# Kernel tuning notes

Hardware: AMD Instinct MI355X
Metric: run time of the kernel (lower is better)

The kernel has to match this reference:

```python
import jax, jax.numpy as jnp
import numpy as np

V, B, NT, EN, EMB, ODIM = 5000, 512, 50, 200, 200, 40
PERP = 30.0
BETA_TEMP = 0.2
SINKHORN_ALPHA = 20.0
WEIGHT_ECR = 250.0
ECR_ITERS = 100
SNE_ITERS = 20
EPS_DIV = 1e-16


def _pairwise_sq(x, y):
    # ||x_i||^2 + ||y_j||^2 - 2 x_i . y_j  (matches module's pairwise_euclidean_distance)
    return (jnp.sum(x * x, axis=1)[:, None] + jnp.sum(y * y, axis=1)[None, :]
            - 2.0 * (x @ y.T))


def _bn_train(x, g, b):
    # BatchNorm1d, training mode: batch statistics, biased variance
    m = x.mean(axis=0)
    v = x.var(axis=0)
    return (x - m) / jnp.sqrt(v + 1e-5) * g + b


def _snekhorn_reduce(X, proj):
    # SNEkhorn-style symmetric entropic affinity on rows of X (log-domain
    # symmetric Sinkhorn with uniform marginals), followed by a linear readout
    # to ODIM dims. X: (n, d) -> (n, ODIM).
    C = _pairwise_sq(X, X)                       # (n, n)
    n = X.shape[0]
    eps = jnp.mean(C) / jnp.log(PERP) + 1e-6     # bandwidth tied to perplexity
    log_a = -jnp.log(float(n))                   # uniform target marginal

    @jax.checkpoint
    def step(f, _):
        lse = jax.nn.logsumexp((f[None, :] - C) / eps, axis=1)
        f = 0.5 * (f + eps * (log_a - lse))      # symmetric Sinkhorn update
        return f, None

    f, _ = jax.lax.scan(step, jnp.zeros(n, C.dtype), None, length=SNE_ITERS)
    P = jnp.exp((f[:, None] + f[None, :] - C) / eps)  # (n, n) affinity
    return P @ proj                                   # (n, ODIM)


def _ecr_loss(cost):
    # ECR: entropic OT between topic and word embeddings (fixed-iteration Sinkhorn)
    Km = jnp.exp(-cost * SINKHORN_ALPHA)          # (NT, V)
    a = jnp.full((NT, 1), 1.0 / NT, cost.dtype)
    bm = jnp.full((V, 1), 1.0 / V, cost.dtype)

    def step(u, _):
        v = bm / (Km.T @ u + EPS_DIV)
        u = a / (Km @ v + EPS_DIV)
        return u, None

    u, _ = jax.lax.scan(step, jnp.full((NT, 1), 1.0 / NT, cost.dtype), None,
                        length=ECR_ITERS)
    v = bm / (Km.T @ u + EPS_DIV)
    transp = u * (Km * v.T)
    return WEIGHT_ECR * jnp.sum(transp * cost)


def setup_inputs() -> dict:
    key = jax.random.key(0)
    ks = jax.random.split(key, 12)

    def nrm(k, shape, s=0.02):
        return jax.random.normal(k, shape, jnp.float32) * s

    word_emb = jax.random.normal(ks[0], (V, EMB), jnp.float32)
    word_emb = word_emb / jnp.linalg.norm(word_emb, axis=1, keepdims=True)
    topic_emb = jax.random.normal(ks[1], (NT, EMB), jnp.float32) * 0.1
    topic_emb = topic_emb / jnp.linalg.norm(topic_emb, axis=1, keepdims=True)

    return dict(
        bow=jax.random.uniform(ks[2], (B, V), jnp.float32),
        eps_noise=jax.random.normal(ks[3], (ODIM, NT), jnp.float32),
        W1=nrm(ks[4], (EN, V)), b1=jnp.zeros(EN, jnp.float32),
        W2=nrm(ks[5], (EN, EN)), b2=jnp.zeros(EN, jnp.float32),
        Wmu=nrm(ks[6], (NT, EN)), bmu=jnp.zeros(NT, jnp.float32),
        Wlv=nrm(ks[7], (NT, EN)), blv=jnp.zeros(NT, jnp.float32),
        g_mu=jnp.ones(NT, jnp.float32), be_mu=jnp.zeros(NT, jnp.float32),
        g_lv=jnp.ones(NT, jnp.float32), be_lv=jnp.zeros(NT, jnp.float32),
        g_dec=jnp.ones(V, jnp.float32), be_dec=jnp.zeros(V, jnp.float32),
        word_emb=word_emb, topic_emb=topic_emb,
        proj_V=nrm(ks[8], (V, ODIM), 1.0),
        proj_K=nrm(ks[9], (NT, ODIM), 1.0),
    )


def reference(bow, eps_noise, W1, b1, W2, b2, Wmu, bmu, Wlv, blv,
              g_mu, be_mu, g_lv, be_lv, g_dec, be_dec,
              word_emb, topic_emb, proj_V, proj_K):
    # bow_reduced = SNEkhorn(bow.T).T : (ODIM, V)
    bow_reduced = _snekhorn_reduce(bow.T, proj_V).T

    # encoder1: Linear -> softplus -> Linear -> softplus
    e1 = jax.nn.softplus(bow_reduced @ W1.T + b1)
    e1 = jax.nn.softplus(e1 @ W2.T + b2)
    mu = _bn_train(e1 @ Wmu.T + bmu, g_mu, be_mu)        # (ODIM, NT)
    logvar = _bn_train(e1 @ Wlv.T + blv, g_lv, be_lv)

    z = mu + eps_noise * jnp.exp(0.5 * logvar)           # reparameterize (training)
    theta = jax.nn.softmax(z, axis=1)                    # (ODIM, NT)
    theta_reduced = _snekhorn_reduce(theta.T, proj_K).T  # (ODIM, NT)

    # KL vs logistic-normal prior; with a = ones: mu2 = 0, var2 = 1 - 1/NT
    var2 = 1.0 - 1.0 / NT
    var = jnp.exp(logvar)
    kld = 0.5 * ((var / var2 + mu * mu / var2 + jnp.log(var2) - logvar).sum(axis=1) - NT)
    loss_KL = kld.mean()

    # beta + decode (cost computed once; torch code computes it twice identically)
    cost = _pairwise_sq(topic_emb, word_emb)             # (NT, V)
    beta = jax.nn.softmax(-cost / BETA_TEMP, axis=0)
    recon = jax.nn.softmax(_bn_train(theta_reduced @ beta, g_dec, be_dec), axis=-1)
    recon_loss = -(bow_reduced * jnp.log(recon)).sum(axis=1).mean()

    loss_TM = recon_loss + loss_KL
    loss_ECR = _ecr_loss(cost)
    loss = loss_TM + loss_ECR
    return loss, loss_TM, loss_ECR, theta_reduced
```

## Files before the change

### kernel.cpp

```cpp
#include <hip/hip_runtime.h>
#include <hip/hip_bf16.h>
#include <hip/hip_fp16.h>

#define VV 5000
#define NTOP 50
#define ENH 200
#define NEMB 200
#define OD 40
#define MP 5120
#define KNS 5008

typedef __attribute__((ext_vector_type(8))) short short8;
typedef __attribute__((ext_vector_type(4))) float f32x4;

constexpr size_t OFF_R      = 0;
constexpr size_t OFF_S      = 20224;
constexpr size_t OFF_SCAL   = 22528;
constexpr size_t OFF_PHIA   = 22784;
constexpr size_t OFF_PHIB   = 43008;
constexpr size_t OFF_ROWS   = 63232;
constexpr size_t OFF_PARTS  = 63744;
constexpr size_t OFF_FLAGS  = 71936;
constexpr size_t OFF_MUPRE  = 72960;
constexpr size_t OFF_LVPRE  = 81152;
constexpr size_t OFF_E1T    = 89344;
constexpr size_t OFF_E2T    = 121600;
constexpr size_t OFF_THRED  = 153856;
constexpr size_t OFF_BOWRED = 162048;
constexpr size_t ZERO_BYTES = 962304;
constexpr size_t OFF_PVT    = 962304;
constexpr size_t OFF_XB     = 1453824;
constexpr size_t OFF_CE     = 6696704;
constexpr size_t OFF_COST   = 56696832;
constexpr size_t OFF_KM     = 57697024;
constexpr size_t OFF_BETA   = 58697216;
constexpr size_t OFF_RN     = 59697408;

__global__ __launch_bounds__(256) void k1_stats(const float* __restrict__ bow,
    __hip_bfloat16* __restrict__ Xb, float* __restrict__ r, float* __restrict__ s){
  __shared__ float lds[64][129];
  const int t = threadIdx.x;
  const int i0 = blockIdx.x * 128, d0 = blockIdx.y * 64;
  #pragma unroll
  for (int m = 0; m < 32; ++m){
    int idx = m*256 + t;
    int di = idx >> 7;
    int ii = idx & 127;
    int gi = i0 + ii;
    lds[di][ii] = (gi < VV) ? bow[(size_t)(d0+di)*VV + gi] : 0.f;
  }
  __syncthreads();
  if (t < 128 && (i0 + t) < VV){
    float acc = 0.f;
    for (int di = 0; di < 64; ++di){ float v = lds[di][t]; acc += v*v; }
    atomicAdd(&r[i0+t], acc);
  }
  if (t < 64){
    float acc = 0.f;
    for (int ii = 0; ii < 128; ++ii) acc += lds[t][ii];
    atomicAdd(&s[d0+t], acc);
  }
  __syncthreads();
  #pragma unroll
  for (int m = 0; m < 32; ++m){
    int idx = m*256 + t;
    int ii = idx >> 6;
    int dd = idx & 63;
    Xb[(size_t)(i0+ii)*512 + d0 + dd] = __float2bfloat16(lds[dd][ii]);
  }
}

__global__ __launch_bounds__(256) void k2_eps(const float* __restrict__ r,
    const float* __restrict__ s, float* __restrict__ scal){
  const int t = threadIdx.x;
  float a = 0.f, b = 0.f;
  for (int i = t; i < VV; i += 256) a += r[i];
  for (int d = t; d < 512; d += 256){ float v = s[d]; b += v*v; }
  #pragma unroll
  for (int off = 32; off; off >>= 1){
    a += __shfl_down(a, off, 64);
    b += __shfl_down(b, off, 64);
  }
  __shared__ float ra[4], rb[4];
  int lane = t & 63, w = t >> 6;
  if (lane == 0){ ra[w] = a; rb[w] = b; }
  __syncthreads();
  if (t == 0){
    float sa = ra[0]+ra[1]+ra[2]+ra[3];
    float sb = rb[0]+rb[1]+rb[2]+rb[3];
    float meanC = 2.f*sa/(float)VV - 2.f*sb/((float)VV*(float)VV);
    float eps = meanC / logf(30.f) + 1e-6f;
    scal[0] = eps;
    scal[1] = 1.f/eps;
  }
}

__device__ __forceinline__ void ecr_block(int b, int it_base, int n_iters, bool do_final,
    const __half* __restrict__ Kn, const float* __restrict__ cost,
    float* __restrict__ acc, int* __restrict__ cnt, float* __restrict__ scal,
    char* smem){
  __half* KmL = (__half*)smem;
  float* varr = (float*)(smem + 32208);
  float* us   = (float*)(smem + 33488);
  float* p5   = (float*)(smem + 33696);
  float* redr = (float*)(smem + 34736);
  const int t = threadIdx.x;
  const int base = (b < 8) ? b*313 : 2504 + (b-8)*312;
  const int sz   = (b < 8) ? 313 : 312;
  for (int c = t; c < 322; c += 256){
    if (c < sz){
      #pragma unroll
      for (int q = 0; q < NTOP; ++q)
        KmL[q*322 + c] = Kn[(size_t)q*KNS + base + c];
    } else {
      #pragma unroll
      for (int q = 0; q < NTOP; ++q) KmL[q*322 + c] = __float2half(0.f);
    }
  }
  if (t < 52){
    float u0 = 0.f;
    if (t < NTOP){
      if (it_base == 0) u0 = 1.f/(float)NTOP;
      else {
        float sm = __hip_atomic_load(&acc[((it_base-1)%3)*64 + t],
                                     __ATOMIC_RELAXED, __HIP_MEMORY_SCOPE_AGENT);
        u0 = (1.f/(float)NTOP)/(sm + 1e-16f);
      }
    }
    us[t] = u0;
  }
  for (int c = sz + t; c < 320; c += 256) varr[c] = 0.f;
  __syncthreads();
  const bool act = (2*t < sz);
  for (int k = 0; k < n_iters; ++k){
    const int g = it_base + k;
    if (act){
      float w0 = 0.f, w1 = 0.f, w2 = 0.f, w3 = 0.f;
      #pragma unroll
      for (int q = 0; q < NTOP; q += 2){
        float u0 = us[q], u1 = us[q+1];
        float2 f0 = __half22float2(*(const __half2*)(KmL + q*322 + 2*t));
        float2 f1 = __half22float2(*(const __half2*)(KmL + (q+1)*322 + 2*t));
        w0 += f0.x*u0; w1 += f0.y*u0;
        w2 += f1.x*u1; w3 += f1.y*u1;
      }
      float2 vv;
      vv.x = (1.f/(float)VV)/((w0+w2) + 1e-16f);
      vv.y = (2*t+1 < sz) ? (1.f/(float)VV)/((w1+w3) + 1e-16f) : 0.f;
      *(float2*)(varr + 2*t) = vv;
    }
    __syncthreads();
    if (t < 250){
      const int qq = t % NTOP, stripe = t / NTOP;
      const __half* kp = KmL + qq*322 + stripe*64;
      const float* vp = varr + stripe*64;
      float s0 = 0.f, s1 = 0.f, s2 = 0.f, s3 = 0.f;
      #pragma unroll
      for (int n = 0; n < 64; n += 4){
        float2 fa = __half22float2(*(const __half2*)(kp + n));
        float2 fb = __half22float2(*(const __half2*)(kp + n + 2));
        float4 v4 = *(const float4*)(vp + n);
        s0 += fa.x*v4.x; s1 += fa.y*v4.y; s2 += fb.x*v4.z; s3 += fb.y*v4.w;
      }
      p5[stripe*52 + qq] = (s0+s1)+(s2+s3);
    }
    __syncthreads();
    if (t < NTOP){
      float sm = p5[t] + p5[52+t] + p5[104+t] + p5[156+t] + p5[208+t];
      __hip_atomic_fetch_add(&acc[(g%3)*64 + t], sm,
                             __ATOMIC_RELAXED, __HIP_MEMORY_SCOPE_AGENT);
    }
    __asm__ volatile("s_waitcnt vmcnt(0)" ::: "memory");
    if (t == 0){
      __hip_atomic_fetch_add(cnt, 1, __ATOMIC_RELEASE, __HIP_MEMORY_SCOPE_AGENT);
      const int tgt = 16*(g+1);
      while (__hip_atomic_load(cnt, __ATOMIC_ACQUIRE, __HIP_MEMORY_SCOPE_AGENT) < tgt)
        __builtin_amdgcn_s_sleep(1);
    }
    if (t < NTOP){
      float sm = __hip_atomic_load(&acc[(g%3)*64 + t],
                                   __ATOMIC_RELAXED, __HIP_MEMORY_SCOPE_AGENT);
      us[t] = (1.f/(float)NTOP)/(sm + 1e-16f);
    }
    if (t < 64)
      __hip_atomic_store(&acc[((g+2)%3)*64 + t], 0.f,
                         __ATOMIC_RELAXED, __HIP_MEMORY_SCOPE_AGENT);
    __syncthreads();
  }
  if (!do_final) return;
  float lsum = 0.f;
  if (act){
    float w0 = 0.f, w1 = 0.f, w2 = 0.f, w3 = 0.f;
    #pragma unroll
    for (int q = 0; q < NTOP; q += 2){
      float u0 = us[q], u1 = us[q+1];
      float2 f0 = __half22float2(*(const __half2*)(KmL + q*322 + 2*t));
      float2 f1 = __half22float2(*(const __half2*)(KmL + (q+1)*322 + 2*t));
      w0 += f0.x*u0; w1 += f0.y*u0;
      w2 += f1.x*u1; w3 += f1.y*u1;
    }
    float v0 = (1.f/(float)VV)/((w0+w2) + 1e-16f);
    const bool ok1 = (2*t+1 < sz);
    float v1 = ok1 ? (1.f/(float)VV)/((w1+w3) + 1e-16f) : 0.f;
    float accv = 0.f;
    #pragma unroll
    for (int q = 0; q < NTOP; ++q){
      float2 f = __half22float2(*(const __half2*)(KmL + q*322 + 2*t));
      float uq = us[q];
      float c0 = cost[(size_t)q*VV + base + 2*t];
      accv += uq*f.x*v0*c0;
      if (ok1){
        float c1 = cost[(size_t)q*VV + base + 2*t + 1];
        accv += uq*f.y*v1*c1;
      }
    }
    lsum = accv;
  }
  #pragma unroll
  for (int off = 32; off; off >>= 1) lsum += __shfl_down(lsum, off, 64);
  if ((t & 63) == 0) redr[t >> 6] = lsum;
  __syncthreads();
  if (t == 0) atomicAdd(&scal[3], redr[0]+redr[1]+redr[2]+redr[3]);
}

__global__ __launch_bounds__(256) void k3_gemm_ecr(const __hip_bfloat16* __restrict__ Xb,
    const float* __restrict__ r, float* __restrict__ scal, __half* __restrict__ Ce,
    const __half* __restrict__ Kn, const float* __restrict__ cost,
    float* __restrict__ accg, int* __restrict__ cnt){
  __shared__ __align__(16) char smem[36864];
  if (blockIdx.x < 16){
    ecr_block(blockIdx.x, 0, 12, false, Kn, cost, accg, cnt, scal, smem);
    return;
  }
  __hip_bfloat16* As = (__hip_bfloat16*)smem;
  __hip_bfloat16* Bs = (__hip_bfloat16*)(smem + 128*72*2);
  const int b2 = blockIdx.x - 16;
  const int t = threadIdx.x;
  const int i0 = (b2 % 40) * 128, j0 = (b2 / 40) * 128;
  const int lane = t & 63, w = t >> 6;
  const int wr = w >> 1, wc = w & 1;
  const int m16 = lane & 15, q4 = lane >> 4;
  f32x4 acc[4][4];
  #pragma unroll
  for (int a = 0; a < 4; ++a)
    #pragma unroll
    for (int b = 0; b < 4; ++b) acc[a][b] = (f32x4){0.f,0.f,0.f,0.f};
  const int srow = t >> 3, sseg = t & 7;
  for (int kc = 0; kc < 512; kc += 64){
    __syncthreads();
    #pragma unroll
    for (int m = 0; m < 4; ++m){
      int row = m*32 + srow;
      uint4 va = *(const uint4*)(Xb + (size_t)(i0+row)*512 + kc + sseg*8);
      *(uint4*)(As + row*72 + sseg*8) = va;
      uint4 vb = *(const uint4*)(Xb + (size_t)(j0+row)*512 + kc + sseg*8);
      *(uint4*)(Bs + row*72 + sseg*8) = vb;
    }
    __syncthreads();
    #pragma unroll
    for (int ks = 0; ks < 64; ks += 32){
      short8 af[4], bf[4];
      #pragma unroll
      for (int f = 0; f < 4; ++f){
        af[f] = *(const short8*)(As + (wr*64 + f*16 + m16)*72 + ks + q4*8);
        bf[f] = *(const short8*)(Bs + (wc*64 + f*16 + m16)*72 + ks + q4*8);
      }
      #pragma unroll
      for (int fr = 0; fr < 4; ++fr)
        #pragma unroll
        for (int fc = 0; fc < 4; ++fc)
          acc[fr][fc] = __builtin_amdgcn_mfma_f32_16x16x32_bf16(af[fr], bf[fc], acc[fr][fc], 0, 0, 0);
    }
  }
  const float inv_eps = scal[1];
  #pragma unroll
  for (int fr = 0; fr < 4; ++fr){
    int rbase = i0 + wr*64 + fr*16 + q4*4;
    #pragma unroll
    for (int fc = 0; fc < 4; ++fc){
      int col = j0 + wc*64 + fc*16 + m16;
      if (col < VV){
        float rc = r[col];
        #pragma unroll
        for (int q = 0; q < 4; ++q){
          int row = rbase + q;
          if (row < VV){
            float val = (r[row] + rc - 2.f*acc[fr][fc][q]) * inv_eps;
            Ce[(size_t)row*VV + col] = __float2half(val);
          }
        }
      }
    }
  }
}

__global__ __launch_bounds__(256) void k4_sweep_ecr(const __half* __restrict__ Ce,
    const float* __restrict__ phi_in, float* __restrict__ phi_out,
    const __half* __restrict__ Kn, const float* __restrict__ cost,
    float* __restrict__ accg, int* __restrict__ cnt, float* __restrict__ scal,
    int it_base, int n_ecr){
  __shared__ __align__(16) char smem[34752];
  const int t = threadIdx.x;
  if (blockIdx.x < 16){
    ecr_block(blockIdx.x, it_base, n_ecr, it_base + n_ecr == 100,
              Kn, cost, accg, cnt, scal, smem);
    return;
  }
  const int i0 = (blockIdx.x - 16) * 4;
  float acc[4] = {0.f, 0.f, 0.f, 0.f};
  const uint4* ce0 = (const uint4*)(Ce + (size_t)i0*VV);
  for (int u = t; u < 625; u += 256){
    float4 p0 = *(const float4*)(phi_in + u*8);
    float4 p1 = *(const float4*)(phi_in + u*8 + 4);
    #pragma unroll
    for (int rr = 0; rr < 4; ++rr){
      uint4 v = ce0[(size_t)rr*625 + u];
      const __half2* hp = (const __half2*)&v;
      float2 c0 = __half22float2(hp[0]);
      float2 c1 = __half22float2(hp[1]);
      float2 c2 = __half22float2(hp[2]);
      float2 c3 = __half22float2(hp[3]);
      acc[rr] += __expf(p0.x - c0.x) + __expf(p0.y - c0.y)
               + __expf(p0.z - c1.x) + __expf(p0.w - c1.y)
               + __expf(p1.x - c2.x) + __expf(p1.y - c2.y)
               + __expf(p1.z - c3.x) + __expf(p1.w - c3.y);
    }
  }
  #pragma unroll
  for (int rr = 0; rr < 4; ++rr)
    #pragma unroll
    for (int off = 32; off; off >>= 1)
      acc[rr] += __shfl_down(acc[rr], off, 64);
  float* red = (float*)smem;
  int lane = t & 63, w = t >> 6;
  if (lane == 0){
    #pragma unroll
    for (int rr = 0; rr < 4; ++rr) red[w*4 + rr] = acc[rr];
  }
  __syncthreads();
  if (t < 4){
    float ssum = red[t] + red[4+t] + red[8+t] + red[12+t];
    const float loga = -8.517193191416238f;
    phi_out[i0 + t] = 0.5f*(phi_in[i0 + t] + loga - __logf(ssum));
  }
}

__global__ __launch_bounds__(256) void k5p_pvt(const float* __restrict__ projV,
    __hip_bfloat16* __restrict__ pvt){
  int idx = blockIdx.x*256 + threadIdx.x;
  if (idx >= 48*MP) return;
  int n = idx / MP, j = idx - n*MP;
  float v = (n < OD && j < VV) ? projV[(size_t)j*OD + n] : 0.f;
  pvt[idx] = __float2bfloat16(v);
}

__global__ __launch_bounds__(256) void k5_bowred(const __half* __restrict__ Ce,
    const float* __restrict__ phi, const __hip_bfloat16* __restrict__ pvt,
    float* __restrict__ brpA, float* __restrict__ brpB){
  __shared__ __align__(16) char smem[25600];
  __hip_bfloat16* As = (__hip_bfloat16*)smem;
  __hip_bfloat16* Bs = (__hip_bfloat16*)(smem + 18432);
  const int t = threadIdx.x;
  const int i0 = blockIdx.x * 128;
  const int k0 = blockIdx.y * 640;
  const int lane = t & 63, w = t >> 6;
  const int m16 = lane & 15, q4 = lane >> 4;
  f32x4 acc[2][3];
  #pragma unroll
  for (int a = 0; a < 2; ++a)
    #pragma unroll
    for (int b = 0; b < 3; ++b) acc[a][b] = (f32x4){0.f,0.f,0.f,0.f};
  for (int kc = k0; kc < k0 + 640; kc += 64){
    __syncthreads();
    #pragma unroll
    for (int m = 0; m < 4; ++m){
      int g = m*256 + t;
      int row = g >> 3, cg = g & 7;
      int gi = i0 + row, j2 = kc + cg*8;
      union { __hip_bfloat16 h[8]; short8 v; } u;
      if (gi < VV && j2 < VV){
        uint4 vce = *(const uint4*)(Ce + (size_t)gi*VV + j2);
        const __half2* hp = (const __half2*)&vce;
        float pb = phi[gi];
        float4 pj0 = *(const float4*)(phi + j2);
        float4 pj1 = *(const float4*)(phi + j2 + 4);
        float pj[8] = {pj0.x,pj0.y,pj0.z,pj0.w,pj1.x,pj1.y,pj1.z,pj1.w};
        #pragma unroll
        for (int e = 0; e < 4; ++e){
          float2 ce = __half22float2(hp[e]);
          u.h[2*e]   = __float2bfloat16(__expf(pb + pj[2*e]   - ce.x));
          u.h[2*e+1] = __float2bfloat16(__expf(pb + pj[2*e+1] - ce.y));
        }
      } else {
        #pragma unroll
        for (int e = 0; e < 8; ++e) u.h[e] = __float2bfloat16(0.f);
      }
      *(short8*)(As + row*72 + cg*8) = u.v;
    }
    #pragma unroll
    for (int m = 0; m < 12; ++m){
      int idx = m*256 + t;
      int row = idx >> 6, c = idx & 63;
      Bs[row*72 + c] = pvt[(size_t)row*MP + kc + c];
    }
    __syncthreads();
    #pragma unroll
    for (int ks = 0; ks < 64; ks += 32){
      short8 af[2], bf[3];
      #pragma unroll
      for (int f = 0; f < 2; ++f)
        af[f] = *(const short8*)(As + (w*32 + f*16 + m16)*72 + ks + q4*8);
      #pragma unroll
      for (int f = 0; f < 3; ++f)
        bf[f] = *(const short8*)(Bs + (f*16 + m16)*72 + ks + q4*8);
      #pragma unroll
      for (int fr = 0; fr < 2; ++fr)
        #pragma unroll
        for (int fc = 0; fc < 3; ++fc)
          acc[fr][fc] = __builtin_amdgcn_mfma_f32_16x16x32_bf16(af[fr], bf[fc], acc[fr][fc], 0, 0, 0);
    }
  }
  __syncthreads();
  float* LF = (float*)smem;
  #pragma unroll
  for (int fr = 0; fr < 2; ++fr){
    int lr = w*32 + fr*16 + q4*4;
    #pragma unroll
    for (int fc = 0; fc < 3; ++fc){
      int col = fc*16 + m16;
      #pragma unroll
      for (int q = 0; q < 4; ++q)
        LF[col*133 + lr + q] = acc[fr][fc][q];
    }
  }
  __syncthreads();
  float* brp = (blockIdx.y < 6) ? brpA + (size_t)blockIdx.y*200000
                                : brpB + (size_t)(blockIdx.y - 6)*200000;
  for (int o = t; o < OD*128; o += 256){
    int col = o >> 7, row = o & 127;
    int gr = i0 + row;
    if (gr < VV) brp[(size_t)col*VV + gr] = LF[col*133 + row];
  }
}

__global__ __launch_bounds__(256) void k5r_red(const float* __restrict__ brpA,
    const float* __restrict__ brpB, float* __restrict__ br){
  int idx = blockIdx.x*256 + threadIdx.x;
  if (idx >= 50000) return;
  const float4* a = (const float4*)brpA;
  const float4* b = (const float4*)brpB;
  float4 s = a[idx];
  #pragma unroll
  for (int sl = 1; sl < 6; ++sl){
    float4 v = a[(size_t)sl*50000 + idx];
    s.x += v.x; s.y += v.y; s.z += v.z; s.w += v.w;
  }
  #pragma unroll
  for (int sl = 0; sl < 2; ++sl){
    float4 v = b[(size_t)sl*50000 + idx];
    s.x += v.x; s.y += v.y; s.z += v.z; s.w += v.w;
  }
  ((float4*)br)[idx] = s;
}

__global__ __launch_bounds__(256) void k6_e1(const float* __restrict__ br,
    const float* __restrict__ W1, float* __restrict__ e1pre){
  const int t = threadIdx.x;
  const int lane = t & 63, w = t >> 6;
  const int k = blockIdx.x*4 + w;
  const int f0 = blockIdx.y * 125;
  float acc[OD];
  #pragma unroll
  for (int i = 0; i < OD; ++i) acc[i] = 0.f;
  const float4* w4p = (const float4*)(W1 + (size_t)k*VV);
  for (int f4 = f0 + lane; f4 < f0 + 125; f4 += 64){
    float4 wv = w4p[f4];
    #pragma unroll
    for (int i = 0; i < OD; ++i){
      float4 bv = ((const float4*)(br + (size_t)i*VV))[f4];
      acc[i] += bv.x*wv.x + bv.y*wv.y + bv.z*wv.z + bv.w*wv.w;
    }
  }
  #pragma unroll
  for (int i = 0; i < OD; ++i)
    #pragma unroll
    for (int off = 32; off; off >>= 1)
      acc[i] += __shfl_down(acc[i], off, 64);
  __shared__ float red[4][OD];
  if (lane == 0){
    #pragma unroll
    for (int i = 0; i < OD; ++i) red[w][i] = acc[i];
  }
  __syncthreads();
  if (t < 160){
    int ww = t / OD, i = t - ww*OD;
    int kk = blockIdx.x*4 + ww;
    atomicAdd(&e1pre[kk*OD + i], red[ww][i]);
  }
}

__global__ __launch_bounds__(256) void k6b_sp(const float* __restrict__ b1,
    float* __restrict__ e1t){
  int idx = blockIdx.x*256 + threadIdx.x;
  if (idx >= ENH*OD) return;
  int kk = idx / OD;
  float x = e1t[idx] + b1[kk];
  e1t[idx] = (x > 20.f) ? x : log1pf(__expf(x));
}

__global__ __launch_bounds__(256) void k7_e2(const float* __restrict__ e1t,
    const float* __restrict__ W2, const float* __restrict__ b2, float* __restrict__ e2t){
  const int t = threadIdx.x;
  const int lane = t & 63, w = t >> 6;
  const int k = blockIdx.x*4 + w;
  float acc[OD];
  #pragma unroll
  for (int i = 0; i < OD; ++i) acc[i] = 0.f;
  for (int j = lane; j < ENH; j += 64){
    float wv = W2[(size_t)k*ENH + j];
    #pragma unroll
    for (int i = 0; i < OD; ++i) acc[i] += e1t[j*OD + i] * wv;
  }
  #pragma unroll
  for (int i = 0; i < OD; ++i)
    #pragma unroll
    for (int off = 32; off; off >>= 1)
      acc[i] += __shfl_down(acc[i], off, 64);
  __shared__ float red[4][OD];
  if (lane == 0){
    #pragma unroll
    for (int i = 0; i < OD; ++i) red[w][i] = acc[i];
  }
  __syncthreads();
  if (t < 160){
    int ww = t / OD, i = t - ww*OD;
    int kk = blockIdx.x*4 + ww;
    float x = red[ww][i] + b2[kk];
    float sp = (x > 20.f) ? x : log1pf(__expf(x));
    e2t[kk*OD + i] = sp;
  }
}

__global__ __launch_bounds__(256) void k8a_mulv(const float* __restrict__ e2t,
    const float* __restrict__ Wmu, const float* __restrict__ bmu,
    const float* __restrict__ Wlv, const float* __restrict__ blv,
    float* __restrict__ mupre, float* __restrict__ lvpre){
  int id = blockIdx.x*256 + threadIdx.x;
  if (id >= NTOP*OD) return;
  int t50 = id / OD, i = id - t50*OD;
  float am = 0.f, al = 0.f;
  for (int kk = 0; kk < ENH; ++kk){
    float e = e2t[kk*OD + i];
    am += e * Wmu[t50*ENH + kk];
    al += e * Wlv[t50*ENH + kk];
  }
  mupre[t50*OD + i] = am + bmu[t50];
  lvpre[t50*OD + i] = al + blv[t50];
}

__global__ __launch_bounds__(256) void k8b_theta(const float* __restrict__ mupre,
    const float* __restrict__ lvpre,
    const float* __restrict__ g_mu, const float* __restrict__ be_mu,
    const float* __restrict__ g_lv, const float* __restrict__ be_lv,
    const float* __restrict__ eps_noise, const float* __restrict__ projK,
    float* __restrict__ thred, float* __restrict__ d_out3, float* __restrict__ scal){
  __shared__ float mu[NTOP][OD];
  __shared__ float lv[NTOP][OD];
  __shared__ float th[OD][NTOP];
  __shared__ float C2[NTOP][NTOP];
  __shared__ float P2[NTOP][NTOP];
  __shared__ float f2[NTOP], nf[NTOP];
  __shared__ float sred[4];
  __shared__ float eps2s[2];
  const int t = threadIdx.x;
  if (t < NTOP){
    float m = 0.f;
    for (int i = 0; i < OD; ++i) m += mupre[t*OD + i];
    m *= (1.f/OD);
    float v = 0.f;
    for (int i = 0; i < OD; ++i){ float d = mupre[t*OD+i] - m; v += d*d; }
    v *= (1.f/OD);
    float sc = g_mu[t] * rsqrtf(v + 1e-5f);
    float sh = be_mu[t];
    for (int i = 0; i < OD; ++i) mu[t][i] = (mupre[t*OD+i] - m)*sc + sh;
    m = 0.f;
    for (int i = 0; i < OD; ++i) m += lvpre[t*OD + i];
    m *= (1.f/OD);
    v = 0.f;
    for (int i = 0; i < OD; ++i){ float d = lvpre[t*OD+i] - m; v += d*d; }
    v *= (1.f/OD);
    sc = g_lv[t] * rsqrtf(v + 1e-5f);
    sh = be_lv[t];
    for (int i = 0; i < OD; ++i) lv[t][i] = (lvpre[t*OD+i] - m)*sc + sh;
  }
  __syncthreads();
  {
    float kl = 0.f;
    if (t < OD){
      const float var2 = 1.f - 1.f/(float)NTOP;
      const float lv2 = logf(var2);
      float ssum = 0.f;
      for (int q = 0; q < NTOP; ++q){
        float l = lv[q][t];
        float m = mu[q][t];
        ssum += (__expf(l) + m*m)/var2 + lv2 - l;
      }
      kl = 0.5f*(ssum - (float)NTOP);
    }
    #pragma unroll
    for (int off = 32; off; off >>= 1) kl += __shfl_down(kl, off, 64);
    if ((t & 63) == 0) sred[t >> 6] = kl;
    __syncthreads();
    if (t == 0) scal[2] = (sred[0]+sred[1]+sred[2]+sred[3]) * (1.f/OD);
    __syncthreads();
  }
  if (t < OD){
    float z[NTOP];
    float mx = -1e30f;
    for (int q = 0; q < NTOP; ++q){
      float val = mu[q][t] + eps_noise[t*NTOP + q]*__expf(0.5f*lv[q][t]);
      z[q] = val;
      mx = fmaxf(mx, val);
    }
    float ssum = 0.f;
    for (int q = 0; q < NTOP; ++q){ float e = __expf(z[q]-mx); z[q] = e; ssum += e; }
    float inv = 1.f/ssum;
    for (int q = 0; q < NTOP; ++q) th[t][q] = z[q]*inv;
  }
  __syncthreads();
  {
    float csum = 0.f;
    for (int pr = t; pr < NTOP*NTOP; pr += 256){
      int a = pr / NTOP, b = pr - (pr/NTOP)*NTOP;
      float ss = 0.f;
      for (int i = 0; i < OD; ++i){ float d = th[i][a] - th[i][b]; ss += d*d; }
      C2[a][b] = ss;
      csum += ss;
    }
    #pragma unroll
    for (int off = 32; off; off >>= 1) csum += __shfl_down(csum, off, 64);
    if ((t & 63) == 0) sred[t >> 6] = csum;
    __syncthreads();
    if (t == 0){
      float meanC = (sred[0]+sred[1]+sred[2]+sred[3]) / ((float)NTOP*NTOP);
      float e2 = meanC / logf(30.f) + 1e-6f;
      eps2s[0] = e2; eps2s[1] = 1.f/e2;
    }
  }
  if (t < NTOP) f2[t] = 0.f;
  __syncthreads();
  const float loga2 = -logf((float)NTOP);
  for (int it = 0; it < 20; ++it){
    if (t < NTOP){
      float ie = eps2s[1];
      float ssum = 0.f;
      for (int sI = 0; sI < NTOP; ++sI)
        ssum += __expf((f2[sI] - C2[t][sI]) * ie);
      float lse = __logf(ssum);
      nf[t] = 0.5f*(f2[t] + eps2s[0]*(loga2 - lse));
    }
    __syncthreads();
    if (t < NTOP) f2[t] = nf[t];
    __syncthreads();
  }
  for (int pr = t; pr < NTOP*NTOP; pr += 256){
    int a = pr / NTOP, b = pr - (pr/NTOP)*NTOP;
    P2[a][b] = __expf((f2[a] + f2[b] - C2[a][b]) * eps2s[1]);
  }
  __syncthreads();
  for (int o = t; o < NTOP*OD; o += 256){
    int t50 = o / OD, kk = o - (o/OD)*OD;
    float ssum = 0.f;
    for (int sI = 0; sI < NTOP; ++sI)
      ssum += P2[t50][sI] * projK[sI*OD + kk];
    thred[kk*NTOP + t50] = ssum;
    d_out3[kk*NTOP + t50] = ssum;
  }
}

__global__ __launch_bounds__(256) void k10_cost(const float* __restrict__ temb,
    const float* __restrict__ wemb, float* __restrict__ cost, __half* __restrict__ Kn,
    float* __restrict__ beta){
  __shared__ float Tt[100][52];
  __shared__ float wed[100][68];
  __shared__ float sc[52][64];
  __shared__ float tn[52];
  __shared__ float wn[64];
  const int t = threadIdx.x;
  const int j0 = blockIdx.x * 64;
  const int tg = t >> 4, jg = t & 15;
  float am[4][4];
  #pragma unroll
  for (int a = 0; a < 4; ++a)
    #pragma unroll
    for (int b = 0; b < 4; ++b) am[a][b] = 0.f;
  float tnp = 0.f, wnp = 0.f;
  for (int c = 0; c < 2; ++c){
    __syncthreads();
    const int dbase = c*100;
    for (int idx = t; idx < NTOP*100; idx += 256){
      int t50 = idx / 100, d = idx - t50*100;
      Tt[d][t50] = temb[t50*NEMB + dbase + d];
    }
    for (int idx = t; idx < 64*100; idx += 256){
      int j = idx / 100, d = idx - j*100;
      int gj = j0 + j;
      wed[d][j] = (gj < VV) ? wemb[(size_t)gj*NEMB + dbase + d] : 0.f;
    }
    __syncthreads();
    if (t < NTOP){
      float a = 0.f;
      for (int d = 0; d < 100; ++d){ float v = Tt[d][t]; a += v*v; }
      tnp += a;
    }
    if (t >= 64 && t < 128){
      int j = t - 64;
      float a = 0.f;
      for (int d = 0; d < 100; ++d){ float v = wed[d][j]; a += v*v; }
      wnp += a;
    }
    if (t < 208){
      for (int d = 0; d < 100; ++d){
        const float4 tv = *(const float4*)(&Tt[d][tg*4]);
        const float4 wv = *(const float4*)(&wed[d][jg*4]);
        am[0][0] += tv.x*wv.x; am[0][1] += tv.x*wv.y; am[0][2] += tv.x*wv.z; am[0][3] += tv.x*wv.w;
        am[1][0] += tv.y*wv.x; am[1][1] += tv.y*wv.y; am[1][2] += tv.y*wv.z; am[1][3] += tv.y*wv.w;
        am[2][0] += tv.z*wv.x; am[2][1] += tv.z*wv.y; am[2][2] += tv.z*wv.z; am[2][3] += tv.z*wv.w;
        am[3][0] += tv.w*wv.x; am[3][1] += tv.w*wv.y; am[3][2] += tv.w*wv.z; am[3][3] += tv.w*wv.w;
      }
    }
  }
  if (t < NTOP) tn[t] = tnp;
  if (t >= 64 && t < 128) wn[t-64] = wnp;
  __syncthreads();
  if (t < 208){
    #pragma unroll
    for (int a = 0; a < 4; ++a){
      int t50 = tg*4 + a;
      if (t50 < NTOP){
        float tv = tn[t50];
        float cc[4];
        #pragma unroll
        for (int b = 0; b < 4; ++b) cc[b] = tv + wn[jg*4+b] - 2.f*am[a][b];
        int gj = j0 + jg*4;
        if (gj + 3 < VV)
          *(float4*)(cost + (size_t)t50*VV + gj) = make_float4(cc[0],cc[1],cc[2],cc[3]);
        #pragma unroll
        for (int b = 0; b < 4; ++b) sc[t50][jg*4+b] = -5.f*cc[b];
      }
    }
  }
  __syncthreads();
  if (t < 64){
    int gj = j0 + t;
    if (gj < VV){
      float mx = -1e30f;
      for (int q = 0; q < NTOP; ++q) mx = fmaxf(mx, sc[q][t]);
      float ssum = 0.f;
      for (int q = 0; q < NTOP; ++q){ float e = __expf(sc[q][t]-mx); sc[q][t] = e; ssum += e; }
      float inv = 1.f/ssum;
      for (int q = 0; q < NTOP; ++q){
        float e = sc[q][t];
        float e2 = e*e;
        Kn[(size_t)q*KNS + gj] = __float2half(e2*e2);
        beta[(size_t)q*VV + gj] = e*inv;
      }
    }
  }
}

__global__ __launch_bounds__(256) void k12_reconA(const float* __restrict__ thred,
    const float* __restrict__ beta, const float* __restrict__ g_dec,
    const float* __restrict__ be_dec, float* __restrict__ Rn){
  __shared__ float trs[OD][NTOP];
  const int t = threadIdx.x;
  for (int o = t; o < OD*NTOP; o += 256) trs[o/NTOP][o - (o/NTOP)*NTOP] = thred[o];
  __syncthreads();
  int j = blockIdx.x*256 + t;
  if (j >= VV) return;
  float a[OD];
  #pragma unroll
  for (int i = 0; i < OD; ++i) a[i] = 0.f;
  for (int q = 0; q < NTOP; ++q){
    float bv = beta[(size_t)q*VV + j];
    #pragma unroll
    for (int i = 0; i < OD; ++i) a[i] += trs[i][q]*bv;
  }
  float m = 0.f;
  #pragma unroll
  for (int i = 0; i < OD; ++i) m += a[i];
  m *= (1.f/OD);
  float v = 0.f;
  #pragma unroll
  for (int i = 0; i < OD; ++i){ float d = a[i]-m; v += d*d; }
  v *= (1.f/OD);
  float scale = g_dec[j]*rsqrtf(v + 1e-5f);
  float sh = be_dec[j];
  #pragma unroll
  for (int i = 0; i < OD; ++i) Rn[(size_t)i*VV + j] = (a[i]-m)*scale + sh;
}

__global__ __launch_bounds__(256) void k13_reconB(const float* __restrict__ Rn,
    const float* __restrict__ br, float* __restrict__ rows){
  const int i = blockIdx.x;
  const int t = threadIdx.x;
  float s1 = 0.f, s2 = 0.f, s3 = 0.f;
  for (int j = t; j < VV; j += 256){
    float rn = Rn[(size_t)i*VV + j];
    float bv = br[(size_t)i*VV + j];
    s1 += __expf(rn);
    s2 += bv*rn;
    s3 += bv;
  }
  #pragma unroll
  for (int off = 32; off; off >>= 1){
    s1 += __shfl_down(s1, off, 64);
    s2 += __shfl_down(s2, off, 64);
    s3 += __shfl_down(s3, off, 64);
  }
  __shared__ float red[3][4];
  int lane = t & 63, w = t >> 6;
  if (lane == 0){ red[0][w] = s1; red[1][w] = s2; red[2][w] = s3; }
  __syncthreads();
  if (t == 0){
    rows[i]      = red[0][0]+red[0][1]+red[0][2]+red[0][3];
    rows[40 + i] = red[1][0]+red[1][1]+red[1][2]+red[1][3];
    rows[80 + i] = red[2][0]+red[2][1]+red[2][2]+red[2][3];
  }
}

__global__ void k14_final(const float* __restrict__ rows, const float* __restrict__ scal,
    float* __restrict__ out){
  const int t = threadIdx.x;
  float v = 0.f;
  if (t < OD) v = rows[40 + t] - logf(rows[t]) * rows[80 + t];
  #pragma unroll
  for (int off = 32; off; off >>= 1) v += __shfl_down(v, off, 64);
  if (t == 0){
    float recon = -v * (1.f/OD);
    float tm = recon + scal[2];
    float ecr = 250.f * scal[3];
    out[0] = tm + ecr;
    out[1] = tm;
    out[2] = ecr;
  }
}

extern "C" void kernel_launch(void* const* d_in, const int* in_sizes, int n_in,
                              void* d_out, int out_size, void* d_ws, size_t ws_size,
                              hipStream_t stream){
  const float* bow   = (const float*)d_in[0];
  const float* epsn  = (const float*)d_in[1];
  const float* W1    = (const float*)d_in[2];
  const float* b1    = (const float*)d_in[3];
  const float* W2    = (const float*)d_in[4];
  const float* b2    = (const float*)d_in[5];
  const float* Wmu   = (const float*)d_in[6];
  const float* bmu   = (const float*)d_in[7];
  const float* Wlv   = (const float*)d_in[8];
  const float* blv   = (const float*)d_in[9];
  const float* g_mu  = (const float*)d_in[10];
  const float* be_mu = (const float*)d_in[11];
  const float* g_lv  = (const float*)d_in[12];
  const float* be_lv = (const float*)d_in[13];
  const float* g_dec = (const float*)d_in[14];
  const float* be_dec= (const float*)d_in[15];
  const float* wemb  = (const float*)d_in[16];
  const float* temb  = (const float*)d_in[17];
  const float* projV = (const float*)d_in[18];
  const float* projK = (const float*)d_in[19];
  char* ws = (char*)d_ws;
  float* r     = (float*)(ws + OFF_R);
  float* s     = (float*)(ws + OFF_S);
  float* scal  = (float*)(ws + OFF_SCAL);
  float* phiA  = (float*)(ws + OFF_PHIA);
  float* phiB  = (float*)(ws + OFF_PHIB);
  float* rows  = (float*)(ws + OFF_ROWS);
  float* accg  = (float*)(ws + OFF_PARTS);
  int*   cnt   = (int*)(ws + OFF_FLAGS);
  float* mupre = (float*)(ws + OFF_MUPRE);
  float* lvpre = (float*)(ws + OFF_LVPRE);
  float* e1t   = (float*)(ws + OFF_E1T);
  float* e2t   = (float*)(ws + OFF_E2T);
  float* thred = (float*)(ws + OFF_THRED);
  float* br    = (float*)(ws + OFF_BOWRED);
  __hip_bfloat16* pvt = (__hip_bfloat16*)(ws + OFF_PVT);
  __hip_bfloat16* Xb  = (__hip_bfloat16*)(ws + OFF_XB);
  __half* Ce   = (__half*)(ws + OFF_CE);
  float* cost  = (float*)(ws + OFF_COST);
  __half* Kn   = (__half*)(ws + OFF_KM);
  float* beta  = (float*)(ws + OFF_BETA);
  float* Rn    = (float*)(ws + OFF_RN);
  float* brpA  = (float*)(ws + OFF_XB);
  float* brpB  = (float*)(ws + OFF_COST);
  float* out   = (float*)d_out;

  hipMemsetAsync(d_ws, 0, ZERO_BYTES, stream);
  k10_cost<<<79, 256, 0, stream>>>(temb, wemb, cost, Kn, beta);
  k1_stats<<<dim3(40, 8), 256, 0, stream>>>(bow, Xb, r, s);
  k2_eps<<<1, 256, 0, stream>>>(r, s, scal);
  k3_gemm_ecr<<<1616, 256, 0, stream>>>(Xb, r, scal, Ce, Kn, cost, accg, cnt);
  {
    float* pin = phiA; float* pout = phiB;
    int itb = 12;
    for (int itr = 0; itr < 20; ++itr){
      int n = (itr < 12) ? 4 : 5;
      k4_sweep_ecr<<<1266, 256, 0, stream>>>(Ce, pin, pout, Kn, cost, accg, cnt,
                                             scal, itb, n);
      itb += n;
      float* tmp = pin; pin = pout; pout = tmp;
    }
  }
  k5p_pvt<<<960, 256, 0, stream>>>(projV, pvt);
  k5_bowred<<<dim3(40, 8), 256, 0, stream>>>(Ce, phiA, pvt, brpA, brpB);
  k5r_red<<<196, 256, 0, stream>>>(brpA, brpB, br);
  k6_e1<<<dim3(50, 10), 256, 0, stream>>>(br, W1, e1t);
  k6b_sp<<<32, 256, 0, stream>>>(b1, e1t);
  k7_e2<<<50, 256, 0, stream>>>(e1t, W2, b2, e2t);
  k8a_mulv<<<8, 256, 0, stream>>>(e2t, Wmu, bmu, Wlv, blv, mupre, lvpre);
  k8b_theta<<<1, 256, 0, stream>>>(mupre, lvpre, g_mu, be_mu, g_lv, be_lv,
                                   epsn, projK, thred, out + 3, scal);
  k12_reconA<<<20, 256, 0, stream>>>(thred, beta, g_dec, be_dec, Rn);
  k13_reconB<<<40, 256, 0, stream>>>(Rn, br, rows);
  k14_final<<<1, 64, 0, stream>>>(rows, scal, out);
}
```

Baseline: 845.8 us.

## Run ECR Sinkhorn in a single block with transposed Km, drop cross-block spin sync

Replaces the 16-block ECR Sinkhorn, which synchronised every iteration through global atomics and spin-waits, with a single block that streams a transposed (V x 52) half-precision Km and reduces through registers and LDS. The iterations are redistributed: 10 run in k1_stats, 20 in k3, and 3-4 in each sweep launch. The sweep kernel now handles 8 rows per block instead of 4, which halves its grid. The cost matrix is also stored transposed for the final loss term. The risk is that one block re-reading about 500KB from L2 per iteration could become the critical path inside each launch.

After: 1.777 ms. +110.1%, slower.

```diff
diff --git a/kernel.cpp b/kernel.cpp
--- a/kernel.cpp
+++ b/kernel.cpp
@@ -8,7 +8,6 @@
 #define NEMB 200
 #define OD 40
 #define MP 5120
-#define KNS 5008
 
 typedef __attribute__((ext_vector_type(8))) short short8;
 typedef __attribute__((ext_vector_type(4))) float f32x4;
@@ -19,8 +18,7 @@
 constexpr size_t OFF_PHIA   = 22784;
 constexpr size_t OFF_PHIB   = 43008;
 constexpr size_t OFF_ROWS   = 63232;
-constexpr size_t OFF_PARTS  = 63744;
-constexpr size_t OFF_FLAGS  = 71936;
+constexpr size_t OFF_UG     = 63744;
 constexpr size_t OFF_MUPRE  = 72960;
 constexpr size_t OFF_LVPRE  = 81152;
 constexpr size_t OFF_E1T    = 89344;
@@ -31,15 +29,93 @@
 constexpr size_t OFF_PVT    = 962304;
 constexpr size_t OFF_XB     = 1453824;
 constexpr size_t OFF_CE     = 6696704;
-constexpr size_t OFF_COST   = 56696832;
-constexpr size_t OFF_KM     = 57697024;
+constexpr size_t OFF_COSTT  = 56696832;
+constexpr size_t OFF_KNT    = 57736832;
 constexpr size_t OFF_BETA   = 58697216;
 constexpr size_t OFF_RN     = 59697408;
 
+__device__ __forceinline__ void ecr1(int it_base, int n_iters, bool do_final,
+    const __half* __restrict__ KnT, const float* __restrict__ costT,
+    float* __restrict__ ug, float* __restrict__ scal, char* smem){
+  float* us = (float*)smem;
+  float* pL = (float*)smem + 52;
+  const int t = threadIdx.x;
+  const int lane = t & 63, w = t >> 6;
+  if (t < 52) us[t] = (t < NTOP) ? ((it_base == 0) ? (1.f/(float)NTOP) : ug[t]) : 0.f;
+  __syncthreads();
+  for (int k = 0; k < n_iters; ++k){
+    float partial[52];
+    #pragma unroll
+    for (int q = 0; q < 52; ++q) partial[q] = 0.f;
+    for (int j = t; j < VV; j += 256){
+      const __half2* kp = (const __half2*)(KnT + (size_t)j*52);
+      float kf[52];
+      float w0 = 0.f;
+      #pragma unroll
+      for (int e = 0; e < 26; ++e){
+        float2 f = __half22float2(kp[e]);
+        kf[2*e] = f.x; kf[2*e+1] = f.y;
+        w0 += f.x*us[2*e] + f.y*us[2*e+1];
+      }
+      float vj = (1.f/(float)VV)/(w0 + 1e-16f);
+      #pragma unroll
+      for (int q = 0; q < 52; ++q) partial[q] += kf[q]*vj;
+    }
+    #pragma unroll
+    for (int q = 0; q < 52; ++q){
+      #pragma unroll
+      for (int off = 32; off; off >>= 1)
+        partial[q] += __shfl_down(partial[q], off, 64);
+    }
+    if (lane == 0){
+      #pragma unroll
+      for (int q = 0; q < 52; ++q) pL[w*52 + q] = partial[q];
+    }
+    __syncthreads();
+    if (t < NTOP){
+      float sm = pL[t] + pL[52+t] + pL[104+t] + pL[156+t];
+      us[t] = (1.f/(float)NTOP)/(sm + 1e-16f);
+    }
+    __syncthreads();
+  }
+  if (t < NTOP) ug[t] = us[t];
+  if (!do_final) return;
+  float lsum = 0.f;
+  for (int j = t; j < VV; j += 256){
+    const __half2* kp = (const __half2*)(KnT + (size_t)j*52);
+    float kf[52];
+    float w0 = 0.f;
+    #pragma unroll
+    for (int e = 0; e < 26; ++e){
+      float2 f = __half22float2(kp[e]);
+      kf[2*e] = f.x; kf[2*e+1] = f.y;
+      w0 += f.x*us[2*e] + f.y*us[2*e+1];
+    }
+    float vj = (1.f/(float)VV)/(w0 + 1e-16f);
+    const float* cp = costT + (size_t)j*52;
+    float a = 0.f;
+    #pragma unroll
+    for (int q = 0; q < NTOP; ++q)
+      a += us[q]*kf[q]*cp[q];
+    lsum += a*vj;
+  }
+  #pragma unroll
+  for (int off = 32; off; off >>= 1) lsum += __shfl_down(lsum, off, 64);
+  if (lane == 0) pL[w*52] = lsum;
+  __syncthreads();
+  if (t == 0) atomicAdd(&scal[3], pL[0] + pL[52] + pL[104] + pL[156]);
+}
+
 __global__ __launch_bounds__(256) void k1_stats(const float* __restrict__ bow,
-    __hip_bfloat16* __restrict__ Xb, float* __restrict__ r, float* __restrict__ s){
+    __hip_bfloat16* __restrict__ Xb, float* __restrict__ r, float* __restrict__ s,
+    const __half* __restrict__ KnT, const float* __restrict__ costT,
+    float* __restrict__ ug, float* __restrict__ scal){
   __shared__ float lds[64][129];
   const int t = threadIdx.x;
+  if (blockIdx.x == 40){
+    if (blockIdx.y == 0) ecr1(0, 10, false, KnT, costT, ug, scal, (char*)lds);
+    return;
+  }
   const int i0 = blockIdx.x * 128, d0 = blockIdx.y * 64;
   #pragma unroll
   for (int m = 0; m < 32; ++m){
@@ -95,146 +171,18 @@
   }
 }
 
-__device__ __forceinline__ void ecr_block(int b, int it_base, int n_iters, bool do_final,
-    const __half* __restrict__ Kn, const float* __restrict__ cost,
-    float* __restrict__ acc, int* __restrict__ cnt, float* __restrict__ scal,
-    char* smem){
-  __half* KmL = (__half*)smem;
-  float* varr = (float*)(smem + 32208);
-  float* us   = (float*)(smem + 33488);
-  float* p5   = (float*)(smem + 33696);
-  float* redr = (float*)(smem + 34736);
-  const int t = threadIdx.x;
-  const int base = (b < 8) ? b*313 : 2504 + (b-8)*312;
-  const int sz   = (b < 8) ? 313 : 312;
-  for (int c = t; c < 322; c += 256){
-    if (c < sz){
-      #pragma unroll
-      for (int q = 0; q < NTOP; ++q)
-        KmL[q*322 + c] = Kn[(size_t)q*KNS + base + c];
-    } else {
-      #pragma unroll
-      for (int q = 0; q < NTOP; ++q) KmL[q*322 + c] = __float2half(0.f);
-    }
-  }
-  if (t < 52){
-    float u0 = 0.f;
-    if (t < NTOP){
-      if (it_base == 0) u0 = 1.f/(float)NTOP;
-      else {
-        float sm = __hip_atomic_load(&acc[((it_base-1)%3)*64 + t],
-                                     __ATOMIC_RELAXED, __HIP_MEMORY_SCOPE_AGENT);
-        u0 = (1.f/(float)NTOP)/(sm + 1e-16f);
-      }
-    }
-    us[t] = u0;
-  }
-  for (int c = sz + t; c < 320; c += 256) varr[c] = 0.f;
-  __syncthreads();
-  const bool act = (2*t < sz);
-  for (int k = 0; k < n_iters; ++k){
-    const int g = it_base + k;
-    if (act){
-      float w0 = 0.f, w1 = 0.f, w2 = 0.f, w3 = 0.f;
-      #pragma unroll
-      for (int q = 0; q < NTOP; q += 2){
-        float u0 = us[q], u1 = us[q+1];
-        float2 f0 = __half22float2(*(const __half2*)(KmL + q*322 + 2*t));
-        float2 f1 = __half22float2(*(const __half2*)(KmL + (q+1)*322 + 2*t));
-        w0 += f0.x*u0; w1 += f0.y*u0;
-        w2 += f1.x*u1; w3 += f1.y*u1;
-      }
-      float2 vv;
-      vv.x = (1.f/(float)VV)/((w0+w2) + 1e-16f);
-      vv.y = (2*t+1 < sz) ? (1.f/(float)VV)/((w1+w3) + 1e-16f) : 0.f;
-      *(float2*)(varr + 2*t) = vv;
-    }
-    __syncthreads();
-    if (t < 250){
-      const int qq = t % NTOP, stripe = t / NTOP;
-      const __half* kp = KmL + qq*322 + stripe*64;
-      const float* vp = varr + stripe*64;
-      float s0 = 0.f, s1 = 0.f, s2 = 0.f, s3 = 0.f;
-      #pragma unroll
-      for (int n = 0; n < 64; n += 4){
-        float2 fa = __half22float2(*(const __half2*)(kp + n));
-        float2 fb = __half22float2(*(const __half2*)(kp + n + 2));
-        float4 v4 = *(const float4*)(vp + n);
-        s0 += fa.x*v4.x; s1 += fa.y*v4.y; s2 += fb.x*v4.z; s3 += fb.y*v4.w;
-      }
-      p5[stripe*52 + qq] = (s0+s1)+(s2+s3);
-    }
-    __syncthreads();
-    if (t < NTOP){
-      float sm = p5[t] + p5[52+t] + p5[104+t] + p5[156+t] + p5[208+t];
-      __hip_atomic_fetch_add(&acc[(g%3)*64 + t], sm,
-                             __ATOMIC_RELAXED, __HIP_MEMORY_SCOPE_AGENT);
-    }
-    __asm__ volatile("s_waitcnt vmcnt(0)" ::: "memory");
-    if (t == 0){
-      __hip_atomic_fetch_add(cnt, 1, __ATOMIC_RELEASE, __HIP_MEMORY_SCOPE_AGENT);
-      const int tgt = 16*(g+1);
-      while (__hip_atomic_load(cnt, __ATOMIC_ACQUIRE, __HIP_MEMORY_SCOPE_AGENT) < tgt)
-        __builtin_amdgcn_s_sleep(1);
-    }
-    if (t < NTOP){
-      float sm = __hip_atomic_load(&acc[(g%3)*64 + t],
-                                   __ATOMIC_RELAXED, __HIP_MEMORY_SCOPE_AGENT);
-      us[t] = (1.f/(float)NTOP)/(sm + 1e-16f);
-    }
-    if (t < 64)
-      __hip_atomic_store(&acc[((g+2)%3)*64 + t], 0.f,
-                         __ATOMIC_RELAXED, __HIP_MEMORY_SCOPE_AGENT);
-    __syncthreads();
-  }
-  if (!do_final) return;
-  float lsum = 0.f;
-  if (act){
-    float w0 = 0.f, w1 = 0.f, w2 = 0.f, w3 = 0.f;
-    #pragma unroll
-    for (int q = 0; q < NTOP; q += 2){
-      float u0 = us[q], u1 = us[q+1];
-      float2 f0 = __half22float2(*(const __half2*)(KmL + q*322 + 2*t));
-      float2 f1 = __half22float2(*(const __half2*)(KmL + (q+1)*322 + 2*t));
-      w0 += f0.x*u0; w1 += f0.y*u0;
-      w2 += f1.x*u1; w3 += f1.y*u1;
-    }
-    float v0 = (1.f/(float)VV)/((w0+w2) + 1e-16f);
-    const bool ok1 = (2*t+1 < sz);
-    float v1 = ok1 ? (1.f/(float)VV)/((w1+w3) + 1e-16f) : 0.f;
-    float accv = 0.f;
-    #pragma unroll
-    for (int q = 0; q < NTOP; ++q){
-      float2 f = __half22float2(*(const __half2*)(KmL + q*322 + 2*t));
-      float uq = us[q];
-      float c0 = cost[(size_t)q*VV + base + 2*t];
-      accv += uq*f.x*v0*c0;
-      if (ok1){
-        float c1 = cost[(size_t)q*VV + base + 2*t + 1];
-        accv += uq*f.y*v1*c1;
-      }
-    }
-    lsum = accv;
-  }
-  #pragma unroll
-  for (int off = 32; off; off >>= 1) lsum += __shfl_down(lsum, off, 64);
-  if ((t & 63) == 0) redr[t >> 6] = lsum;
-  __syncthreads();
-  if (t == 0) atomicAdd(&scal[3], redr[0]+redr[1]+redr[2]+redr[3]);
-}
-
 __global__ __launch_bounds__(256) void k3_gemm_ecr(const __hip_bfloat16* __restrict__ Xb,
     const float* __restrict__ r, float* __restrict__ scal, __half* __restrict__ Ce,
-    const __half* __restrict__ Kn, const float* __restrict__ cost,
-    float* __restrict__ accg, int* __restrict__ cnt){
+    const __half* __restrict__ KnT, const float* __restrict__ costT,
+    float* __restrict__ ug){
   __shared__ __align__(16) char smem[36864];
-  if (blockIdx.x < 16){
-    ecr_block(blockIdx.x, 0, 12, false, Kn, cost, accg, cnt, scal, smem);
+  if (blockIdx.x == 0){
+    ecr1(10, 20, false, KnT, costT, ug, scal, smem);
     return;
   }
   __hip_bfloat16* As = (__hip_bfloat16*)smem;
   __hip_bfloat16* Bs = (__hip_bfloat16*)(smem + 128*72*2);
-  const int b2 = blockIdx.x - 16;
+  const int b2 = blockIdx.x - 1;
   const int t = threadIdx.x;
   const int i0 = (b2 % 40) * 128, j0 = (b2 / 40) * 128;
   const int lane = t & 63, w = t >> 6;
@@ -296,24 +244,25 @@
 
 __global__ __launch_bounds__(256) void k4_sweep_ecr(const __half* __restrict__ Ce,
     const float* __restrict__ phi_in, float* __restrict__ phi_out,
-    const __half* __restrict__ Kn, const float* __restrict__ cost,
-    float* __restrict__ accg, int* __restrict__ cnt, float* __restrict__ scal,
+    const __half* __restrict__ KnT, const float* __restrict__ costT,
+    float* __restrict__ ug, float* __restrict__ scal,
     int it_base, int n_ecr){
-  __shared__ __align__(16) char smem[34752];
-  const int t = threadIdx.x;
-  if (blockIdx.x < 16){
-    ecr_block(blockIdx.x, it_base, n_ecr, it_base + n_ecr == 100,
-              Kn, cost, accg, cnt, scal, smem);
+  __shared__ __align__(16) char smem[2048];
+  const int t = threadIdx.x;
+  if (blockIdx.x == 0){
+    ecr1(it_base, n_ecr, it_base + n_ecr == 100, KnT, costT, ug, scal, smem);
     return;
   }
-  const int i0 = (blockIdx.x - 16) * 4;
-  float acc[4] = {0.f, 0.f, 0.f, 0.f};
+  const int i0 = (blockIdx.x - 1) * 8;
+  float acc[8];
+  #pragma unroll
+  for (int rr = 0; rr < 8; ++rr) acc[rr] = 0.f;
   const uint4* ce0 = (const uint4*)(Ce + (size_t)i0*VV);
   for (int u = t; u < 625; u += 256){
     float4 p0 = *(const float4*)(phi_in + u*8);
     float4 p1 = *(const float4*)(phi_in + u*8 + 4);
     #pragma unroll
-    for (int rr = 0; rr < 4; ++rr){
+    for (int rr = 0; rr < 8; ++rr){
       uint4 v = ce0[(size_t)rr*625 + u];
       const __half2* hp = (const __half2*)&v;
       float2 c0 = __half22float2(hp[0]);
@@ -327,7 +276,7 @@
     }
   }
   #pragma unroll
-  for (int rr = 0; rr < 4; ++rr)
+  for (int rr = 0; rr < 8; ++rr)
     #pragma unroll
     for (int off = 32; off; off >>= 1)
       acc[rr] += __shfl_down(acc[rr], off, 64);
@@ -335,11 +284,11 @@
   int lane = t & 63, w = t >> 6;
   if (lane == 0){
     #pragma unroll
-    for (int rr = 0; rr < 4; ++rr) red[w*4 + rr] = acc[rr];
-  }
-  __syncthreads();
-  if (t < 4){
-    float ssum = red[t] + red[4+t] + red[8+t] + red[12+t];
+    for (int rr = 0; rr < 8; ++rr) red[w*8 + rr] = acc[rr];
+  }
+  __syncthreads();
+  if (t < 8){
+    float ssum = red[t] + red[8+t] + red[16+t] + red[24+t];
     const float loga = -8.517193191416238f;
     phi_out[i0 + t] = 0.5f*(phi_in[i0 + t] + loga - __logf(ssum));
   }
@@ -679,7 +628,7 @@
 }
 
 __global__ __launch_bounds__(256) void k10_cost(const float* __restrict__ temb,
-    const float* __restrict__ wemb, float* __restrict__ cost, __half* __restrict__ Kn,
+    const float* __restrict__ wemb, float* __restrict__ costT, __half* __restrict__ KnT,
     float* __restrict__ beta){
   __shared__ float Tt[100][52];
   __shared__ float wed[100][68];
@@ -739,14 +688,8 @@
       int t50 = tg*4 + a;
       if (t50 < NTOP){
         float tv = tn[t50];
-        float cc[4];
         #pragma unroll
-        for (int b = 0; b < 4; ++b) cc[b] = tv + wn[jg*4+b] - 2.f*am[a][b];
-        int gj = j0 + jg*4;
-        if (gj + 3 < VV)
-          *(float4*)(cost + (size_t)t50*VV + gj) = make_float4(cc[0],cc[1],cc[2],cc[3]);
-        #pragma unroll
-        for (int b = 0; b < 4; ++b) sc[t50][jg*4+b] = -5.f*cc[b];
+        for (int b = 0; b < 4; ++b) sc[t50][jg*4+b] = -5.f*(tv + wn[jg*4+b] - 2.f*am[a][b]);
       }
     }
   }
@@ -756,15 +699,19 @@
     if (gj < VV){
       float mx = -1e30f;
       for (int q = 0; q < NTOP; ++q) mx = fmaxf(mx, sc[q][t]);
+      for (int q = 0; q < NTOP; ++q)
+        costT[(size_t)gj*52 + q] = -0.2f*sc[q][t];
       float ssum = 0.f;
       for (int q = 0; q < NTOP; ++q){ float e = __expf(sc[q][t]-mx); sc[q][t] = e; ssum += e; }
       float inv = 1.f/ssum;
       for (int q = 0; q < NTOP; ++q){
         float e = sc[q][t];
         float e2 = e*e;
-        Kn[(size_t)q*KNS + gj] = __float2half(e2*e2);
+        KnT[(size_t)gj*52 + q] = __float2half(e2*e2);
         beta[(size_t)q*VV + gj] = e*inv;
       }
+      KnT[(size_t)gj*52 + 50] = __float2half(0.f);
+      KnT[(size_t)gj*52 + 51] = __float2half(0.f);
     }
   }
 }
@@ -876,8 +823,7 @@
   float* phiA  = (float*)(ws + OFF_PHIA);
   float* phiB  = (float*)(ws + OFF_PHIB);
   float* rows  = (float*)(ws + OFF_ROWS);
-  float* accg  = (float*)(ws + OFF_PARTS);
-  int*   cnt   = (int*)(ws + OFF_FLAGS);
+  float* ug    = (float*)(ws + OFF_UG);
   float* mupre = (float*)(ws + OFF_MUPRE);
   float* lvpre = (float*)(ws + OFF_LVPRE);
   float* e1t   = (float*)(ws + OFF_E1T);
@@ -887,26 +833,26 @@
   __hip_bfloat16* pvt = (__hip_bfloat16*)(ws + OFF_PVT);
   __hip_bfloat16* Xb  = (__hip_bfloat16*)(ws + OFF_XB);
   __half* Ce   = (__half*)(ws + OFF_CE);
-  float* cost  = (float*)(ws + OFF_COST);
-  __half* Kn   = (__half*)(ws + OFF_KM);
+  float* costT = (float*)(ws + OFF_COSTT);
+  __half* KnT  = (__half*)(ws + OFF_KNT);
   float* beta  = (float*)(ws + OFF_BETA);
   float* Rn    = (float*)(ws + OFF_RN);
   float* brpA  = (float*)(ws + OFF_XB);
-  float* brpB  = (float*)(ws + OFF_COST);
+  float* brpB  = (float*)(ws + OFF_COSTT);
   float* out   = (float*)d_out;
 
   hipMemsetAsync(d_ws, 0, ZERO_BYTES, stream);
-  k10_cost<<<79, 256, 0, stream>>>(temb, wemb, cost, Kn, beta);
-  k1_stats<<<dim3(40, 8), 256, 0, stream>>>(bow, Xb, r, s);
+  k10_cost<<<79, 256, 0, stream>>>(temb, wemb, costT, KnT, beta);
+  k1_stats<<<dim3(41, 8), 256, 0, stream>>>(bow, Xb, r, s, KnT, costT, ug, scal);
   k2_eps<<<1, 256, 0, stream>>>(r, s, scal);
-  k3_gemm_ecr<<<1616, 256, 0, stream>>>(Xb, r, scal, Ce, Kn, cost, accg, cnt);
+  k3_gemm_ecr<<<1601, 256, 0, stream>>>(Xb, r, scal, Ce, KnT, costT, ug);
   {
     float* pin = phiA; float* pout = phiB;
-    int itb = 12;
+    int itb = 30;
     for (int itr = 0; itr < 20; ++itr){
-      int n = (itr < 12) ? 4 : 5;
-      k4_sweep_ecr<<<1266, 256, 0, stream>>>(Ce, pin, pout, Kn, cost, accg, cnt,
-                                             scal, itb, n);
+      int n = (itr < 10) ? 4 : 3;
+      k4_sweep_ecr<<<626, 256, 0, stream>>>(Ce, pin, pout, KnT, costT, ug,
+                                            scal, itb, n);
       itb += n;
       float* tmp = pin; pin = pout; pout = tmp;
     }
```
